# Kernel tuning notes

Measured on AMD Instinct MI355X. Metric: run time of the kernel, lower is better.

## Reference

```python
import jax, jax.numpy as jnp
import numpy as np

N, D, H = 50000, 128, 2        # nodes, hidden_size(=ffn_size=out_channels), heads
E = 800000                      # edges
C = D                           # per-head out_channels (PyG TransformerConv)
EPS = 1e-5

def layer_norm(x, g, b):
    mu = jnp.mean(x, axis=-1, keepdims=True)
    var = jnp.mean((x - mu) ** 2, axis=-1, keepdims=True)
    return (x - mu) / jnp.sqrt(var + EPS) * g + b

def setup_inputs() -> dict:
    key = jax.random.key(0)
    ks = jax.random.split(key, 16)
    s_in = 1.0 / np.sqrt(D)
    s_ffn = 1.0 / np.sqrt(D)
    return {
        "x": jax.random.normal(ks[0], (N, D), jnp.float32),
        "edge_index": jax.random.randint(ks[1], (2, E), 0, N, jnp.int64),
        "ln1_g": jnp.ones((D,), jnp.float32),
        "ln1_b": jnp.zeros((D,), jnp.float32),
        "Wq": jax.random.normal(ks[2], (D, H * C), jnp.float32) * s_in,
        "bq": jnp.zeros((H * C,), jnp.float32),
        "Wk": jax.random.normal(ks[3], (D, H * C), jnp.float32) * s_in,
        "bk": jnp.zeros((H * C,), jnp.float32),
        "Wv": jax.random.normal(ks[4], (D, H * C), jnp.float32) * s_in,
        "bv": jnp.zeros((H * C,), jnp.float32),
        "Wskip": jax.random.normal(ks[5], (D, C), jnp.float32) * s_in,
        "bskip": jnp.zeros((C,), jnp.float32),
        "ln2_g": jnp.ones((D,), jnp.float32),
        "ln2_b": jnp.zeros((D,), jnp.float32),
        "W1": jax.random.normal(ks[6], (D, D), jnp.float32) * s_ffn,
        "b1": jnp.zeros((D,), jnp.float32),
        "W2": jax.random.normal(ks[7], (D, D), jnp.float32) * s_ffn,
        "b2": jnp.zeros((D,), jnp.float32),
    }

def reference(x, edge_index, ln1_g, ln1_b, Wq, bq, Wk, bk, Wv, bv,
              Wskip, bskip, ln2_g, ln2_b, W1, b1, W2, b2):
    src, dst = edge_index[0], edge_index[1]  # messages flow src(j) -> dst(i)
    n = x.shape[0]

    # --- self-attention block (pre-norm) ---
    y = layer_norm(x, ln1_g, ln1_b)
    q = (y @ Wq + bq).reshape(n, H, C)
    k = (y @ Wk + bk).reshape(n, H, C)
    v = (y @ Wv + bv).reshape(n, H, C)

    # per-edge attention logits [E, H]
    alpha = jnp.einsum('ehc,ehc->eh', q[dst], k[src]) / jnp.sqrt(jnp.float32(C))
    # softmax over incoming edges of each dst node
    m = jax.ops.segment_max(alpha, dst, num_segments=n)          # [N, H]
    p = jnp.exp(alpha - m[dst])                                  # [E, H]
    denom = jax.ops.segment_sum(p, dst, num_segments=n)          # [N, H]
    a = p / denom[dst]                                           # [E, H]

    attn = jax.ops.segment_sum(a[:, :, None] * v[src], dst, num_segments=n)  # [N,H,C]
    out = attn.mean(axis=1) + (y @ Wskip + bskip)  # concat=False mean + root skip
    x = x + out  # residual (dropout is identity at eval)

    # --- FFN block (pre-norm) ---
    h = layer_norm(x, ln2_g, ln2_b)
    h = jax.nn.gelu(h @ W1 + b1, approximate=False) @ W2 + b2
    return x + h
```

## Files before the change

kernel.cpp:

```cpp
#include <hip/hip_runtime.h>
#include <hip/hip_bf16.h>
#include <math.h>


typedef unsigned short u16;
using short8 = __attribute__((ext_vector_type(8))) short;
using f32x4  = __attribute__((ext_vector_type(4))) float;
using f32x2  = __attribute__((ext_vector_type(2))) float;

__device__ __forceinline__ float bf2f(u16 u) {
    return __uint_as_float(((unsigned int)u) << 16);
}
__device__ __forceinline__ u16 f2bf(float f) {
    __hip_bfloat16 h = __float2bfloat16(f);
    return __builtin_bit_cast(u16, h);
}
__device__ __forceinline__ float bfe(short8 v, int j) {
    return bf2f((u16)v[j]);
}
__device__ __forceinline__ void fp8x4_to_f32(int w, float* out) {
    f32x2 lo = __builtin_amdgcn_cvt_pk_f32_fp8(w, false);
    f32x2 hi = __builtin_amdgcn_cvt_pk_f32_fp8(w, true);
    out[0] = lo[0]; out[1] = lo[1]; out[2] = hi[0]; out[3] = hi[1];
}
__device__ __forceinline__ unsigned pack_fp8x4(float4 f) {
    unsigned w = 0;
    w = (unsigned)__builtin_amdgcn_cvt_pk_fp8_f32(f.x, f.y, (int)w, false);
    w = (unsigned)__builtin_amdgcn_cvt_pk_fp8_f32(f.z, f.w, (int)w, true);
    return w;
}

__global__ __launch_bounds__(256) void fused_prep_ln(
    const float* __restrict__ x, const float* __restrict__ ln1g,
    const float* __restrict__ ln1b,
    const float* __restrict__ Wq, const float* __restrict__ Wk,
    const float* __restrict__ Wv, const float* __restrict__ Ws,
    const float* __restrict__ W1, const float* __restrict__ W2,
    const float* __restrict__ bq, const float* __restrict__ bk,
    const float* __restrict__ bv, const float* __restrict__ bs,
    u16* __restrict__ wt, float* __restrict__ bc,
    u16* __restrict__ y, int* __restrict__ cnt, int* __restrict__ rank, int n,
    const int* __restrict__ edst, int e, int histBlocks)
{
    if (blockIdx.x < (unsigned)histBlocks) {
        int stride = histBlocks * 256;
        for (int i = blockIdx.x * 256 + threadIdx.x; i < e; i += stride)
            rank[i] = atomicAdd(&cnt[edst[i]], 1);
        return;
    }
    int gsz = (gridDim.x - histBlocks) * 256;
    int gtid = (blockIdx.x - histBlocks) * 256 + threadIdx.x;

    for (int i = gtid; i < 147456 + 896; i += gsz) {
        if (i < 147456) {
            const float* W; int N; int base;
            if      (i <  32768) { W = Wq; N = 256; base = 0; }
            else if (i <  65536) { W = Wk; N = 256; base = 32768; }
            else if (i <  98304) { W = Wv; N = 256; base = 65536; }
            else if (i < 114688) { W = Ws; N = 128; base = 98304; }
            else if (i < 131072) { W = W1; N = 128; base = 114688; }
            else                 { W = W2; N = 128; base = 131072; }
            int j = i - base;
            int nIdx = j >> 7, k = j & 127;
            wt[i] = f2bf(W[(size_t)k * N + nIdx]);
        } else {
            int j = i - 147456;
            float v;
            if      (j < 256) v = bq[j];
            else if (j < 512) v = bk[j - 256];
            else if (j < 768) v = bv[j - 512];
            else              v = bs[j - 768];
            bc[j] = v;
        }
    }
    int lane = threadIdx.x & 63;
    int gw = gtid >> 6, nw = gsz >> 6;
    for (int row = gw; row < n; row += nw) {
        size_t base = (size_t)row * 128;
        float v0 = x[base + lane];
        float v1 = x[base + 64 + lane];
        float s1 = v0 + v1, s2 = v0 * v0 + v1 * v1;
        for (int o = 1; o <= 32; o <<= 1) {
            s1 += __shfl_xor(s1, o);
            s2 += __shfl_xor(s2, o);
        }
        float mu = s1 * (1.f / 128.f);
        float var = s2 * (1.f / 128.f) - mu * mu;
        float rstd = rsqrtf(var + 1e-5f);
        y[base + lane]      = f2bf((v0 - mu) * rstd * ln1g[lane] + ln1b[lane]);
        y[base + 64 + lane] = f2bf((v1 - mu) * rstd * ln1g[64 + lane] + ln1b[64 + lane]);
    }
}

__global__ __launch_bounds__(256) void scan_block_sum(const int* __restrict__ cnt,
                                                      int* __restrict__ bsum, int n) {
    __shared__ int s[256];
    int idx = blockIdx.x * 256 + threadIdx.x;
    s[threadIdx.x] = (idx < n) ? cnt[idx] : 0;
    __syncthreads();
    for (int o = 128; o > 0; o >>= 1) {
        if (threadIdx.x < o) s[threadIdx.x] += s[threadIdx.x + o];
        __syncthreads();
    }
    if (threadIdx.x == 0) bsum[blockIdx.x] = s[0];
}
__global__ __launch_bounds__(256) void scan_partials(const int* __restrict__ bsum,
                                                     int* __restrict__ bsumex, int nb) {
    __shared__ int s[256];
    int t = threadIdx.x;
    int v = (t < nb) ? bsum[t] : 0;
    s[t] = v;
    __syncthreads();
    for (int o = 1; o < 256; o <<= 1) {
        int add = (t >= o) ? s[t - o] : 0;
        __syncthreads();
        s[t] += add;
        __syncthreads();
    }
    bsumex[t] = s[t] - v;
}
__global__ __launch_bounds__(256) void scan_write(const int* __restrict__ cnt,
                                                  const int* __restrict__ bsumex,
                                                  int* __restrict__ rowptr,
                                                  int n, int etot) {
    __shared__ int s[256];
    int t = threadIdx.x;
    int idx = blockIdx.x * 256 + t;
    int v = (idx < n) ? cnt[idx] : 0;
    s[t] = v;
    __syncthreads();
    for (int o = 1; o < 256; o <<= 1) {
        int add = (t >= o) ? s[t - o] : 0;
        __syncthreads();
        s[t] += add;
        __syncthreads();
    }
    if (idx < n) rowptr[idx] = bsumex[blockIdx.x] + s[t] - v;
    if (idx == 0) rowptr[n] = etot;
}

__global__ __launch_bounds__(256, 6) void qkv_gemm(
    const u16* __restrict__ A, const u16* __restrict__ Bt,
    const float* __restrict__ bias, u16* __restrict__ qkv,
    float* __restrict__ skip, int n,
    const int* __restrict__ dst, const int* __restrict__ src,
    const int* __restrict__ rank, const int* __restrict__ rowptr,
    int* __restrict__ esrc, int e, int scatBlocks)
{
    __shared__ float epi[4][32 * 33];
    if (blockIdx.x < (unsigned)scatBlocks) {
        int stride = scatBlocks * 256;
        int i = blockIdx.x * 256 + threadIdx.x;
        for (; i + 3 * stride < e; i += 4 * stride) {
            int i1 = i + stride, i2 = i + 2 * stride, i3 = i + 3 * stride;
            int d0 = dst[i],  d1 = dst[i1], d2 = dst[i2], d3 = dst[i3];
            int r0 = rank[i], r1 = rank[i1], r2 = rank[i2], r3 = rank[i3];
            int s0 = src[i],  s1 = src[i1], s2 = src[i2], s3 = src[i3];
            int p0 = rowptr[d0], p1 = rowptr[d1], p2 = rowptr[d2], p3 = rowptr[d3];
            esrc[p0 + r0] = s0; esrc[p1 + r1] = s1;
            esrc[p2 + r2] = s2; esrc[p3 + r3] = s3;
        }
        for (; i < e; i += stride)
            esrc[rowptr[dst[i]] + rank[i]] = src[i];
        return;
    }
    int bid = blockIdx.x - scatBlocks;
    int wc = threadIdx.x >> 6, lane = threadIdx.x & 63;
    int r0 = bid * 32;
    int lm = lane & 15, quad = lane >> 4;

    int ar0 = r0 + lm;       if (ar0 > n - 1) ar0 = n - 1;
    int ar1 = r0 + 16 + lm;  if (ar1 > n - 1) ar1 = n - 1;
    const u16* aB0 = A + (size_t)ar0 * 128 + quad * 8;
    const u16* aB1 = A + (size_t)ar1 * 128 + quad * 8;
    short8 a0_0 = *(const short8*)(aB0 + 0);
    short8 a0_1 = *(const short8*)(aB0 + 32);
    short8 a0_2 = *(const short8*)(aB0 + 64);
    short8 a0_3 = *(const short8*)(aB0 + 96);
    short8 a1_0 = *(const short8*)(aB1 + 0);
    short8 a1_1 = *(const short8*)(aB1 + 32);
    short8 a1_2 = *(const short8*)(aB1 + 64);
    short8 a1_3 = *(const short8*)(aB1 + 96);
    asm volatile("" : "+v"(a0_0), "+v"(a0_1), "+v"(a0_2), "+v"(a0_3),
                      "+v"(a1_0), "+v"(a1_1), "+v"(a1_2), "+v"(a1_3));

    int rr = lane & 31, hh = lane >> 5;
    int row = r0 + rr;
    bool rowOk = row < n;
    float* ep = epi[wc];

    for (int by = 0; by < 7; ++by) {
        int c0 = by * 128;
        const u16* bBase = Bt + (size_t)(c0 + wc * 32 + lm) * 128 + quad * 8;
        f32x4 acc[2][2] = {};
#pragma unroll
        for (int kx = 0; kx < 4; ++kx) {
            short8 a0 = (kx == 0) ? a0_0 : (kx == 1) ? a0_1 : (kx == 2) ? a0_2 : a0_3;
            short8 a1 = (kx == 0) ? a1_0 : (kx == 1) ? a1_1 : (kx == 2) ? a1_2 : a1_3;
#pragma unroll
            for (int j = 0; j < 2; ++j) {
                short8 bj = *(const short8*)(bBase + (size_t)j * 16 * 128 + kx * 32);
                acc[0][j] = __builtin_amdgcn_mfma_f32_16x16x32_bf16(a0, bj, acc[0][j], 0, 0, 0);
                acc[1][j] = __builtin_amdgcn_mfma_f32_16x16x32_bf16(a1, bj, acc[1][j], 0, 0, 0);
            }
        }
#pragma unroll
        for (int j = 0; j < 2; ++j) {
            float bv = bias[c0 + wc * 32 + j * 16 + lm];
#pragma unroll
            for (int rt = 0; rt < 2; ++rt)
#pragma unroll
                for (int i2 = 0; i2 < 4; ++i2)
                    ep[(rt * 16 + quad * 4 + i2) * 33 + j * 16 + lm]
                        = acc[rt][j][i2] + bv;
        }
        if (rowOk) {
            const float* ws = ep + rr * 33 + hh * 16;
            int colW = wc * 32 + hh * 16;
            if (c0 < 256) {
                u16* dp = qkv + (size_t)row * 640 + c0 + colW;
                short8 o0, o1;
#pragma unroll
                for (int jj = 0; jj < 8; ++jj) {
                    o0[jj] = (short)f2bf(ws[jj]);
                    o1[jj] = (short)f2bf(ws[8 + jj]);
                }
                *(short8*)(dp + 0) = o0;
                *(short8*)(dp + 8) = o1;
            } else if (c0 < 512) {
                unsigned char* kb = (unsigned char*)qkv + (size_t)row * 1280
                                    + 512 + (c0 - 256) + colW;
                uint4 o;
                o.x = pack_fp8x4(make_float4(ws[0],  ws[1],  ws[2],  ws[3]));
                o.y = pack_fp8x4(make_float4(ws[4],  ws[5],  ws[6],  ws[7]));
                o.z = pack_fp8x4(make_float4(ws[8],  ws[9],  ws[10], ws[11]));
                o.w = pack_fp8x4(make_float4(ws[12], ws[13], ws[14], ws[15]));
                *(uint4*)kb = o;
            } else if (c0 < 768) {
                u16* dp = qkv + (size_t)row * 640 + 384 + (c0 - 512) + colW;
                short8 o0, o1;
#pragma unroll
                for (int jj = 0; jj < 8; ++jj) {
                    o0[jj] = (short)f2bf(ws[jj]);
                    o1[jj] = (short)f2bf(ws[8 + jj]);
                }
                *(short8*)(dp + 0) = o0;
                *(short8*)(dp + 8) = o1;
            } else {
                float* dp = skip + (size_t)row * 128 + colW;
#pragma unroll
                for (int m2 = 0; m2 < 4; ++m2)
                    *(float4*)(dp + m2 * 4) = *(const float4*)(ws + m2 * 4);
            }
        }
    }
}

__global__ __launch_bounds__(256) void attn_kernel(
    const u16* __restrict__ qkv, const int* __restrict__ rowptr,
    const int* __restrict__ esrc, const float* __restrict__ x,
    float* __restrict__ sx, const float* __restrict__ g2,
    const float* __restrict__ b2, u16* __restrict__ y, int n)
{
    int wid = threadIdx.x >> 6, lane = threadIdx.x & 63;
    int i = blockIdx.x * 4 + wid;
    if (i >= n) return;
    int slot = lane >> 5;
    int sub  = lane & 15;
    int colOff = ((lane >> 4) & 1) * 128 + sub * 8;

    const float scale = 0.08838834764831845f;
    short8 q8 = *(const short8*)(qkv + (size_t)i * 640 + colOff);
    float qf[8];
#pragma unroll
    for (int j = 0; j < 8; ++j) qf[j] = bfe(q8, j) * scale;

    int beg = rowptr[i], end = rowptr[i + 1];
    float l = 0.f;
    float acc[8] = {};

    int t = beg + slot;
    for (; t + 6 < end; t += 8) {
        int s0 = esrc[t], s1 = esrc[t + 2], s2 = esrc[t + 4], s3 = esrc[t + 6];
        const u16* n0 = qkv + (size_t)s0 * 640;
        const u16* n1 = qkv + (size_t)s1 * 640;
        const u16* n2 = qkv + (size_t)s2 * 640;
        const u16* n3 = qkv + (size_t)s3 * 640;
        uint2 kw0 = *(const uint2*)((const unsigned char*)(n0 + 256) + colOff);
        uint2 kw1 = *(const uint2*)((const unsigned char*)(n1 + 256) + colOff);
        uint2 kw2 = *(const uint2*)((const unsigned char*)(n2 + 256) + colOff);
        uint2 kw3 = *(const uint2*)((const unsigned char*)(n3 + 256) + colOff);
        short8 v0 = *(const short8*)(n0 + 384 + colOff);
        short8 v1 = *(const short8*)(n1 + 384 + colOff);
        short8 v2 = *(const short8*)(n2 + 384 + colOff);
        short8 v3 = *(const short8*)(n3 + 384 + colOff);
        float k0f[8], k1f[8], k2f[8], k3f[8];
        fp8x4_to_f32((int)kw0.x, k0f); fp8x4_to_f32((int)kw0.y, k0f + 4);
        fp8x4_to_f32((int)kw1.x, k1f); fp8x4_to_f32((int)kw1.y, k1f + 4);
        fp8x4_to_f32((int)kw2.x, k2f); fp8x4_to_f32((int)kw2.y, k2f + 4);
        fp8x4_to_f32((int)kw3.x, k3f); fp8x4_to_f32((int)kw3.y, k3f + 4);
        float d0 = 0.f, d1 = 0.f, d2 = 0.f, d3 = 0.f;
#pragma unroll
        for (int j = 0; j < 8; ++j) {
            d0 += qf[j] * k0f[j];
            d1 += qf[j] * k1f[j];
            d2 += qf[j] * k2f[j];
            d3 += qf[j] * k3f[j];
        }
#pragma unroll
        for (int o = 1; o <= 8; o <<= 1) {
            d0 += __shfl_xor(d0, o);
            d1 += __shfl_xor(d1, o);
            d2 += __shfl_xor(d2, o);
            d3 += __shfl_xor(d3, o);
        }
        float w0 = __expf(d0), w1 = __expf(d1);
        float w2 = __expf(d2), w3 = __expf(d3);
        l += w0 + w1 + w2 + w3;
#pragma unroll
        for (int j = 0; j < 8; ++j)
            acc[j] += w0 * bfe(v0, j) + w1 * bfe(v1, j)
                    + w2 * bfe(v2, j) + w3 * bfe(v3, j);
    }
    for (; t < end; t += 2) {
        int s0 = esrc[t];
        const u16* n0 = qkv + (size_t)s0 * 640;
        uint2 kw0 = *(const uint2*)((const unsigned char*)(n0 + 256) + colOff);
        short8 v0 = *(const short8*)(n0 + 384 + colOff);
        float k0f[8];
        fp8x4_to_f32((int)kw0.x, k0f); fp8x4_to_f32((int)kw0.y, k0f + 4);
        float d0 = 0.f;
#pragma unroll
        for (int j = 0; j < 8; ++j) d0 += qf[j] * k0f[j];
#pragma unroll
        for (int o = 1; o <= 8; o <<= 1) d0 += __shfl_xor(d0, o);
        float w0 = __expf(d0);
        l += w0;
#pragma unroll
        for (int j = 0; j < 8; ++j) acc[j] += w0 * bfe(v0, j);
    }

    l += __shfl_xor(l, 32);
    float inv = (l > 0.f) ? (1.f / l) : 0.f;
#pragma unroll
    for (int j = 0; j < 8; ++j) {
        acc[j] = (acc[j] + __shfl_xor(acc[j], 32)) * inv;
        acc[j] = 0.5f * (acc[j] + __shfl_xor(acc[j], 16));
    }

    if (lane < 16) {
        size_t base = (size_t)i * 128 + sub * 8;
        float4 xv0 = *(const float4*)(x + base);
        float4 xv1 = *(const float4*)(x + base + 4);
        float4 sk0 = *(const float4*)(sx + base);
        float4 sk1 = *(const float4*)(sx + base + 4);
        float r[8];
        r[0] = xv0.x + sk0.x + acc[0]; r[1] = xv0.y + sk0.y + acc[1];
        r[2] = xv0.z + sk0.z + acc[2]; r[3] = xv0.w + sk0.w + acc[3];
        r[4] = xv1.x + sk1.x + acc[4]; r[5] = xv1.y + sk1.y + acc[5];
        r[6] = xv1.z + sk1.z + acc[6]; r[7] = xv1.w + sk1.w + acc[7];
        *(float4*)(sx + base)     = make_float4(r[0], r[1], r[2], r[3]);
        *(float4*)(sx + base + 4) = make_float4(r[4], r[5], r[6], r[7]);
        float s1 = 0.f, s2 = 0.f;
#pragma unroll
        for (int j = 0; j < 8; ++j) { s1 += r[j]; s2 += r[j] * r[j]; }
#pragma unroll
        for (int o = 1; o <= 8; o <<= 1) {
            s1 += __shfl_xor(s1, o);
            s2 += __shfl_xor(s2, o);
        }
        float mu = s1 * (1.f / 128.f);
        float var = s2 * (1.f / 128.f) - mu * mu;
        float rstd = rsqrtf(var + 1e-5f);
        short8 o8;
#pragma unroll
        for (int j = 0; j < 8; ++j)
            o8[j] = (short)f2bf((r[j] - mu) * rstd * g2[sub * 8 + j] + b2[sub * 8 + j]);
        *(short8*)(y + base) = o8;
    }
}

__global__ __launch_bounds__(256) void ffn_kernel(
    const u16* __restrict__ y2, const u16* __restrict__ W1T,
    const float* __restrict__ b1, const u16* __restrict__ W2T,
    const float* __restrict__ b2, const float* __restrict__ x2,
    float* __restrict__ out, int n)
{
    __shared__ u16 t1[64 * 136];
    int wid = threadIdx.x >> 6, lane = threadIdx.x & 63;
    int lm = lane & 15, quad = lane >> 4;
    int r0 = blockIdx.x * 64 + wid * 16;

    const u16* aBase = y2 + (size_t)(r0 + lm) * 128 + quad * 8;
    f32x4 acc[8] = {};
#pragma unroll
    for (int kk = 0; kk < 128; kk += 32) {
        short8 a0 = *(const short8*)(aBase + kk);
#pragma unroll
        for (int j = 0; j < 8; ++j) {
            short8 bj = *(const short8*)(W1T + (size_t)(j * 16 + lm) * 128 + quad * 8 + kk);
            acc[j] = __builtin_amdgcn_mfma_f32_16x16x32_bf16(a0, bj, acc[j], 0, 0, 0);
        }
    }
#pragma unroll
    for (int j = 0; j < 8; ++j) {
        int col = j * 16 + lm;
        float bv = b1[col];
#pragma unroll
        for (int i2 = 0; i2 < 4; ++i2) {
            int rl = wid * 16 + quad * 4 + i2;
            float v = acc[j][i2] + bv;
            v = 0.5f * v * (1.f + erff(v * 0.70710678118654752f));
            t1[rl * 136 + col] = f2bf(v);
        }
    }
    __syncthreads();

    f32x4 acc2[8] = {};
#pragma unroll
    for (int kk = 0; kk < 128; kk += 32) {
        short8 a0 = *(const short8*)(t1 + (wid * 16 + lm) * 136 + quad * 8 + kk);
#pragma unroll
        for (int j = 0; j < 8; ++j) {
            short8 bj = *(const short8*)(W2T + (size_t)(j * 16 + lm) * 128 + quad * 8 + kk);
            acc2[j] = __builtin_amdgcn_mfma_f32_16x16x32_bf16(a0, bj, acc2[j], 0, 0, 0);
        }
    }
#pragma unroll
    for (int j = 0; j < 8; ++j) {
        int col = j * 16 + lm;
        float bv = b2[col];
#pragma unroll
        for (int i2 = 0; i2 < 4; ++i2) {
            int row = r0 + quad * 4 + i2;
            if (row >= n) continue;
            size_t ob = (size_t)row * 128 + col;
            out[ob] = acc2[j][i2] + bv + x2[ob];
        }
    }
}

extern "C" void kernel_launch(void* const* d_in, const int* in_sizes, int n_in,
                              void* d_out, int out_size, void* d_ws, size_t ws_size,
                              hipStream_t stream)
{
    const float* x    = (const float*)d_in[0];
    const int*   ei   = (const int*)d_in[1];

    int n = in_sizes[0] / 128;
    int e = in_sizes[1] / 2;
    const int* src  = ei;
    const int* dstp = ei + e;

    char* w = (char*)d_ws;
    size_t off = 0;
    auto alloc = [&](size_t bytes) -> void* {
        void* p = w + off;
        off = (off + bytes + 255) & ~(size_t)255;
        return p;
    };
    u16*   y    = (u16*)alloc((size_t)n * 128 * 2);
    u16*   qkv  = (u16*)alloc((size_t)n * 640 * 2);
    float* sx   = (float*)alloc((size_t)n * 128 * 4);
    u16*   wt   = (u16*)alloc((size_t)147456 * 2);
    float* bc   = (float*)alloc(896 * 4);
    int* cnt    = (int*)alloc((size_t)n * 4);
    int* rankA  = (int*)alloc((size_t)e * 4);
    int* rowptr = (int*)alloc(((size_t)n + 1) * 4);
    int* esrc   = (int*)alloc((size_t)e * 4);
    int* bsum   = (int*)alloc(1024);
    int* bsumex = (int*)alloc(1024);

    int gr   = (n + 63) / 64;
    int gr32 = (n + 31) / 32;
    int nb   = (n + 255) / 256;
    int scatBlocks = 1024;
    int histBlocks = 512;

    hipMemsetAsync(cnt, 0, (size_t)n * sizeof(int), stream);
    fused_prep_ln<<<2048 + histBlocks, 256, 0, stream>>>(
        x, (const float*)d_in[2], (const float*)d_in[3],
        (const float*)d_in[4], (const float*)d_in[6], (const float*)d_in[8],
        (const float*)d_in[10], (const float*)d_in[14], (const float*)d_in[16],
        (const float*)d_in[5], (const float*)d_in[7], (const float*)d_in[9],
        (const float*)d_in[11], wt, bc, y, cnt, rankA, n, dstp, e, histBlocks);
    scan_block_sum<<<nb, 256, 0, stream>>>(cnt, bsum, n);
    scan_partials<<<1, 256, 0, stream>>>(bsum, bsumex, nb);
    scan_write<<<nb, 256, 0, stream>>>(cnt, bsumex, rowptr, n, e);
    qkv_gemm<<<scatBlocks + gr32, 256, 0, stream>>>(
        y, wt, bc, qkv, sx, n, dstp, src, rankA, rowptr, esrc, e, scatBlocks);
    attn_kernel<<<(n + 3) / 4, 256, 0, stream>>>(qkv, rowptr, esrc, x, sx,
                                                 (const float*)d_in[12],
                                                 (const float*)d_in[13], y, n);
    ffn_kernel<<<gr, 256, 0, stream>>>(y, wt + 114688, (const float*)d_in[15],
                                       wt + 131072, (const float*)d_in[17],
                                       sx, (float*)d_out, n);
}
```

Measured before the change: 369.8 us.

## Store V in fp8 and interleave K/V per node for single 16-byte gathers

V is now quantized to fp8 like K, and K and V are laid out interleaved per head in a separate 512-byte-per-node buffer. Each lane then fetches its 8 K values and 8 V values with one 16-byte load instead of an 8-byte and a 16-byte load. Q moves to its own bf16 buffer. The aim is to halve the gathered V bytes and cut the number of random memory transactions in the edge loop, at the cost of lower precision in the attention values.

```diff
diff --git a/kernel.cpp b/kernel.cpp
--- a/kernel.cpp
+++ b/kernel.cpp
@@ -141,7 +141,8 @@
 
 __global__ __launch_bounds__(256, 6) void qkv_gemm(
     const u16* __restrict__ A, const u16* __restrict__ Bt,
-    const float* __restrict__ bias, u16* __restrict__ qkv,
+    const float* __restrict__ bias, u16* __restrict__ qbuf,
+    unsigned char* __restrict__ kv,
     float* __restrict__ skip, int n,
     const int* __restrict__ dst, const int* __restrict__ src,
     const int* __restrict__ rank, const int* __restrict__ rowptr,
@@ -218,7 +219,7 @@
             const float* ws = ep + rr * 33 + hh * 16;
             int colW = wc * 32 + hh * 16;
             if (c0 < 256) {
-                u16* dp = qkv + (size_t)row * 640 + c0 + colW;
+                u16* dp = qbuf + (size_t)row * 256 + c0 + colW;
                 short8 o0, o1;
 #pragma unroll
                 for (int jj = 0; jj < 8; ++jj) {
@@ -228,24 +229,27 @@
                 *(short8*)(dp + 0) = o0;
                 *(short8*)(dp + 8) = o1;
             } else if (c0 < 512) {
-                unsigned char* kb = (unsigned char*)qkv + (size_t)row * 1280
-                                    + 512 + (c0 - 256) + colW;
-                uint4 o;
-                o.x = pack_fp8x4(make_float4(ws[0],  ws[1],  ws[2],  ws[3]));
-                o.y = pack_fp8x4(make_float4(ws[4],  ws[5],  ws[6],  ws[7]));
-                o.z = pack_fp8x4(make_float4(ws[8],  ws[9],  ws[10], ws[11]));
-                o.w = pack_fp8x4(make_float4(ws[12], ws[13], ws[14], ws[15]));
-                *(uint4*)kb = o;
+                int kc = (c0 - 256) + colW;
+                int h = kc >> 7, c = kc & 127;
+                unsigned char* kb = kv + (size_t)row * 512 + h * 256 + (c >> 3) * 16;
+                uint2 o0, o1;
+                o0.x = pack_fp8x4(make_float4(ws[0],  ws[1],  ws[2],  ws[3]));
+                o0.y = pack_fp8x4(make_float4(ws[4],  ws[5],  ws[6],  ws[7]));
+                o1.x = pack_fp8x4(make_float4(ws[8],  ws[9],  ws[10], ws[11]));
+                o1.y = pack_fp8x4(make_float4(ws[12], ws[13], ws[14], ws[15]));
+                *(uint2*)kb = o0;
+                *(uint2*)(kb + 16) = o1;
             } else if (c0 < 768) {
-                u16* dp = qkv + (size_t)row * 640 + 384 + (c0 - 512) + colW;
-                short8 o0, o1;
-#pragma unroll
-                for (int jj = 0; jj < 8; ++jj) {
-                    o0[jj] = (short)f2bf(ws[jj]);
-                    o1[jj] = (short)f2bf(ws[8 + jj]);
-                }
-                *(short8*)(dp + 0) = o0;
-                *(short8*)(dp + 8) = o1;
+                int vc = (c0 - 512) + colW;
+                int h = vc >> 7, c = vc & 127;
+                unsigned char* vb = kv + (size_t)row * 512 + h * 256 + (c >> 3) * 16 + 8;
+                uint2 o0, o1;
+                o0.x = pack_fp8x4(make_float4(ws[0],  ws[1],  ws[2],  ws[3]));
+                o0.y = pack_fp8x4(make_float4(ws[4],  ws[5],  ws[6],  ws[7]));
+                o1.x = pack_fp8x4(make_float4(ws[8],  ws[9],  ws[10], ws[11]));
+                o1.y = pack_fp8x4(make_float4(ws[12], ws[13], ws[14], ws[15]));
+                *(uint2*)vb = o0;
+                *(uint2*)(vb + 16) = o1;
             } else {
                 float* dp = skip + (size_t)row * 128 + colW;
 #pragma unroll
@@ -257,7 +261,8 @@
 }
 
 __global__ __launch_bounds__(256) void attn_kernel(
-    const u16* __restrict__ qkv, const int* __restrict__ rowptr,
+    const u16* __restrict__ qbuf, const unsigned char* __restrict__ kv,
+    const int* __restrict__ rowptr,
     const int* __restrict__ esrc, const float* __restrict__ x,
     float* __restrict__ sx, const float* __restrict__ g2,
     const float* __restrict__ b2, u16* __restrict__ y, int n)
@@ -267,10 +272,12 @@
     if (i >= n) return;
     int slot = lane >> 5;
     int sub  = lane & 15;
-    int colOff = ((lane >> 4) & 1) * 128 + sub * 8;
+    int head = (lane >> 4) & 1;
+    int colOff = head * 128 + sub * 8;
+    int kvOff  = head * 256 + sub * 16;
 
     const float scale = 0.08838834764831845f;
-    short8 q8 = *(const short8*)(qkv + (size_t)i * 640 + colOff);
+    short8 q8 = *(const short8*)(qbuf + (size_t)i * 256 + colOff);
     float qf[8];
 #pragma unroll
     for (int j = 0; j < 8; ++j) qf[j] = bfe(q8, j) * scale;
@@ -282,23 +289,20 @@
     int t = beg + slot;
     for (; t + 6 < end; t += 8) {
         int s0 = esrc[t], s1 = esrc[t + 2], s2 = esrc[t + 4], s3 = esrc[t + 6];
-        const u16* n0 = qkv + (size_t)s0 * 640;
-        const u16* n1 = qkv + (size_t)s1 * 640;
-        const u16* n2 = qkv + (size_t)s2 * 640;
-        const u16* n3 = qkv + (size_t)s3 * 640;
-        uint2 kw0 = *(const uint2*)((const unsigned char*)(n0 + 256) + colOff);
-        uint2 kw1 = *(const uint2*)((const unsigned char*)(n1 + 256) + colOff);
-        uint2 kw2 = *(const uint2*)((const unsigned char*)(n2 + 256) + colOff);
-        uint2 kw3 = *(const uint2*)((const unsigned char*)(n3 + 256) + colOff);
-        short8 v0 = *(const short8*)(n0 + 384 + colOff);
-        short8 v1 = *(const short8*)(n1 + 384 + colOff);
-        short8 v2 = *(const short8*)(n2 + 384 + colOff);
-        short8 v3 = *(const short8*)(n3 + 384 + colOff);
+        uint4 kv0 = *(const uint4*)(kv + (size_t)s0 * 512 + kvOff);
+        uint4 kv1 = *(const uint4*)(kv + (size_t)s1 * 512 + kvOff);
+        uint4 kv2 = *(const uint4*)(kv + (size_t)s2 * 512 + kvOff);
+        uint4 kv3 = *(const uint4*)(kv + (size_t)s3 * 512 + kvOff);
         float k0f[8], k1f[8], k2f[8], k3f[8];
-        fp8x4_to_f32((int)kw0.x, k0f); fp8x4_to_f32((int)kw0.y, k0f + 4);
-        fp8x4_to_f32((int)kw1.x, k1f); fp8x4_to_f32((int)kw1.y, k1f + 4);
-        fp8x4_to_f32((int)kw2.x, k2f); fp8x4_to_f32((int)kw2.y, k2f + 4);
-        fp8x4_to_f32((int)kw3.x, k3f); fp8x4_to_f32((int)kw3.y, k3f + 4);
+        float v0f[8], v1f[8], v2f[8], v3f[8];
+        fp8x4_to_f32((int)kv0.x, k0f); fp8x4_to_f32((int)kv0.y, k0f + 4);
+        fp8x4_to_f32((int)kv1.x, k1f); fp8x4_to_f32((int)kv1.y, k1f + 4);
+        fp8x4_to_f32((int)kv2.x, k2f); fp8x4_to_f32((int)kv2.y, k2f + 4);
+        fp8x4_to_f32((int)kv3.x, k3f); fp8x4_to_f32((int)kv3.y, k3f + 4);
+        fp8x4_to_f32((int)kv0.z, v0f); fp8x4_to_f32((int)kv0.w, v0f + 4);
+        fp8x4_to_f32((int)kv1.z, v1f); fp8x4_to_f32((int)kv1.w, v1f + 4);
+        fp8x4_to_f32((int)kv2.z, v2f); fp8x4_to_f32((int)kv2.w, v2f + 4);
+        fp8x4_to_f32((int)kv3.z, v3f); fp8x4_to_f32((int)kv3.w, v3f + 4);
         float d0 = 0.f, d1 = 0.f, d2 = 0.f, d3 = 0.f;
 #pragma unroll
         for (int j = 0; j < 8; ++j) {
@@ -319,16 +323,14 @@
         l += w0 + w1 + w2 + w3;
 #pragma unroll
         for (int j = 0; j < 8; ++j)
-            acc[j] += w0 * bfe(v0, j) + w1 * bfe(v1, j)
-                    + w2 * bfe(v2, j) + w3 * bfe(v3, j);
+            acc[j] += w0 * v0f[j] + w1 * v1f[j] + w2 * v2f[j] + w3 * v3f[j];
     }
     for (; t < end; t += 2) {
         int s0 = esrc[t];
-        const u16* n0 = qkv + (size_t)s0 * 640;
-        uint2 kw0 = *(const uint2*)((const unsigned char*)(n0 + 256) + colOff);
-        short8 v0 = *(const short8*)(n0 + 384 + colOff);
-        float k0f[8];
-        fp8x4_to_f32((int)kw0.x, k0f); fp8x4_to_f32((int)kw0.y, k0f + 4);
+        uint4 kv0 = *(const uint4*)(kv + (size_t)s0 * 512 + kvOff);
+        float k0f[8], v0f[8];
+        fp8x4_to_f32((int)kv0.x, k0f); fp8x4_to_f32((int)kv0.y, k0f + 4);
+        fp8x4_to_f32((int)kv0.z, v0f); fp8x4_to_f32((int)kv0.w, v0f + 4);
         float d0 = 0.f;
 #pragma unroll
         for (int j = 0; j < 8; ++j) d0 += qf[j] * k0f[j];
@@ -337,7 +339,7 @@
         float w0 = __expf(d0);
         l += w0;
 #pragma unroll
-        for (int j = 0; j < 8; ++j) acc[j] += w0 * bfe(v0, j);
+        for (int j = 0; j < 8; ++j) acc[j] += w0 * v0f[j];
     }
 
     l += __shfl_xor(l, 32);
@@ -460,7 +462,8 @@
         return p;
     };
     u16*   y    = (u16*)alloc((size_t)n * 128 * 2);
-    u16*   qkv  = (u16*)alloc((size_t)n * 640 * 2);
+    u16*   qbuf = (u16*)alloc((size_t)n * 256 * 2);
+    unsigned char* kvb = (unsigned char*)alloc((size_t)n * 512);
     float* sx   = (float*)alloc((size_t)n * 128 * 4);
     u16*   wt   = (u16*)alloc((size_t)147456 * 2);
     float* bc   = (float*)alloc(896 * 4);
@@ -488,8 +491,8 @@
     scan_partials<<<1, 256, 0, stream>>>(bsum, bsumex, nb);
     scan_write<<<nb, 256, 0, stream>>>(cnt, bsumex, rowptr, n, e);
     qkv_gemm<<<scatBlocks + gr32, 256, 0, stream>>>(
-        y, wt, bc, qkv, sx, n, dstp, src, rankA, rowptr, esrc, e, scatBlocks);
-    attn_kernel<<<(n + 3) / 4, 256, 0, stream>>>(qkv, rowptr, esrc, x, sx,
+        y, wt, bc, qbuf, kvb, sx, n, dstp, src, rankA, rowptr, esrc, e, scatBlocks);
+    attn_kernel<<<(n + 3) / 4, 256, 0, stream>>>(qbuf, kvb, rowptr, esrc, x, sx,
                                                  (const float*)d_in[12],
                                                  (const float*)d_in[13], y, n);
     ffn_kernel<<<gr, 256, 0, stream>>>(y, wt + 114688, (const float*)d_in[15],
```

After: 359.7 us. 1.03x faster.
